# Kernel tuning notes

Measured on AMD Instinct MI355X. Metric: run time of the kernel, lower is better.

Reference implementation:

```python
import jax, jax.numpy as jnp
import numpy as np

B, S, D_IN, D_OUT = 4, 2048, 1024, 1024


def setup_inputs() -> dict:
    key = jax.random.key(0)
    k1, k2, k3, k4 = jax.random.split(key, 4)
    scale = 1.0 / np.sqrt(D_IN)
    return {
        "x": jax.random.normal(k1, (B, S, D_IN), dtype=jnp.float32),
        # torch nn.Linear weights have shape [d_out, d_in]
        "Wq": jax.random.normal(k2, (D_OUT, D_IN), dtype=jnp.float32) * scale,
        "Wk": jax.random.normal(k3, (D_OUT, D_IN), dtype=jnp.float32) * scale,
        "Wv": jax.random.normal(k4, (D_OUT, D_IN), dtype=jnp.float32) * scale,
    }


def reference(x, Wq, Wk, Wv):
    # Linear projections (torch Linear: y = x @ W.T), no bias
    q = jnp.einsum('bsd,od->bso', x, Wq)
    k = jnp.einsum('bsd,od->bso', x, Wk)
    v = jnp.einsum('bsd,od->bso', x, Wv)
    s = q.shape[1]
    scores = jnp.einsum('bqd,bkd->bqk', q, k)  # [B, S, S]
    causal = jnp.tril(jnp.ones((s, s), dtype=bool))  # True = keep
    scores = jnp.where(causal[None], scores, -jnp.inf)
    scale = jnp.asarray(k.shape[-1], scores.dtype) ** 0.5
    weights = jax.nn.softmax(scores / scale, axis=-1)
    return jnp.einsum('bqk,bkd->bqd', weights, v)
```

## Files before the change

kernel.cpp:

```cpp
#include <hip/hip_runtime.h>

#define BATCH 4
#define SEQ   2048
#define DIM   1024
#define MTOT  (BATCH * SEQ)
#define BK    32

typedef __bf16 bf16x8 __attribute__((ext_vector_type(8)));
typedef float  f32x4  __attribute__((ext_vector_type(4)));

__device__ __forceinline__ void gl_lds16(const __bf16* g, __bf16* l) {
    __builtin_amdgcn_global_load_lds(
        (const __attribute__((address_space(1))) void*)g,
        (__attribute__((address_space(3))) void*)l,
        16, 0, 0);
}

__global__ __launch_bounds__(256) void cvt_all_kernel(
    const float* __restrict__ x,  const float* __restrict__ w0,
    const float* __restrict__ w1, const float* __restrict__ w2,
    __bf16* __restrict__ xd, __bf16* __restrict__ d0,
    __bf16* __restrict__ d1, __bf16* __restrict__ d2)
{
    const int bid = blockIdx.x;
    const float* s;
    __bf16* d;
    int base;
    if (bid < 4096)      { s = x;  d = xd; base = bid; }
    else if (bid < 4608) { s = w0; d = d0; base = bid - 4096; }
    else if (bid < 5120) { s = w1; d = d1; base = bid - 4608; }
    else                 { s = w2; d = d2; base = bid - 5120; }
    const int i = (base * 256 + threadIdx.x) * 8;
    const float4 a = *(const float4*)(s + i);
    const float4 b = *(const float4*)(s + i + 4);
    bf16x8 o;
    o[0] = (__bf16)a.x; o[1] = (__bf16)a.y; o[2] = (__bf16)a.z; o[3] = (__bf16)a.w;
    o[4] = (__bf16)b.x; o[5] = (__bf16)b.y; o[6] = (__bf16)b.z; o[7] = (__bf16)b.w;
    *(bf16x8*)(d + i) = o;
}

__device__ __forceinline__ void gemm_core(
    const __bf16* __restrict__ A, size_t lda,
    const __bf16* __restrict__ Bm, size_t ldb,
    int m0, int n0, int kTiles,
    __bf16* lA, __bf16* lB,
    f32x4 (&acc)[4][4])
{
    const int tid  = threadIdx.x;
    const int lane = tid & 63;
    const int wave = tid >> 6;
    const int wm = (wave >> 1) << 6;
    const int wn = (wave & 1) << 6;

#pragma unroll
    for (int i = 0; i < 4; ++i)
#pragma unroll
        for (int j = 0; j < 4; ++j)
            acc[i][j] = (f32x4){0.f, 0.f, 0.f, 0.f};

    for (int kt = 0; kt < kTiles; ++kt) {
        const int k0 = kt << 5;
        __syncthreads();
#pragma unroll
        for (int it = 0; it < 2; ++it) {
            const int f   = tid + (it << 8);
            const int row = f >> 2;
            const int col = (f & 3) << 3;
            gl_lds16(A  + (size_t)(m0 + row) * lda + (size_t)(k0 + col), lA + f * 8);
            gl_lds16(Bm + (size_t)(n0 + row) * ldb + (size_t)(k0 + col), lB + f * 8);
        }
        __syncthreads();

        bf16x8 af[4], bfr[4];
#pragma unroll
        for (int i = 0; i < 4; ++i) {
            af[i]  = *(const bf16x8*)(lA + (size_t)(wm + i * 16 + (lane & 15)) * BK + ((lane >> 4) << 3));
            bfr[i] = *(const bf16x8*)(lB + (size_t)(wn + i * 16 + (lane & 15)) * BK + ((lane >> 4) << 3));
        }
#pragma unroll
        for (int i = 0; i < 4; ++i)
#pragma unroll
            for (int j = 0; j < 4; ++j)
                acc[i][j] = __builtin_amdgcn_mfma_f32_16x16x32_bf16(af[i], bfr[j], acc[i][j], 0, 0, 0);
    }
}

__device__ __forceinline__ void store_tile_bf16(
    f32x4 (&acc)[4][4], __bf16* scratch, bool transpose, float scale,
    __bf16* dst, size_t ldo, size_t r0, size_t c0,
    bool expMask = false, bool diag = false)
{
    const int tid  = threadIdx.x;
    const int lane = tid & 63;
    const int wave = tid >> 6;
    const int wm = (wave >> 1) << 6, wn = (wave & 1) << 6;
    const int quad = lane >> 4;
    const int ln15 = lane & 15;

#pragma unroll
    for (int p = 0; p < 4; ++p) {
        __syncthreads();
        if (!transpose) {
            if (wm == ((p >> 1) << 6)) {
#pragma unroll
                for (int ih = 0; ih < 2; ++ih) {
                    const int i = ((p & 1) << 1) + ih;
                    const int lr = ih * 16 + quad * 4;
#pragma unroll
                    for (int j = 0; j < 4; ++j)
#pragma unroll
                        for (int r = 0; r < 4; ++r) {
                            const int lm = wm + ((p & 1) << 5) + lr + r;
                            const int ln = wn + j * 16 + ln15;
                            float v = acc[i][j][r] * scale;
                            if (expMask) {
                                v = (!diag || ln <= lm) ? __expf(v) : 0.f;
                            }
                            scratch[(lr + r) * 136 + wn + j * 16 + ln15] = (__bf16)v;
                        }
                }
            }
        } else {
            if (wn == ((p >> 1) << 6)) {
#pragma unroll
                for (int jh = 0; jh < 2; ++jh) {
                    const int j = ((p & 1) << 1) + jh;
                    const int lr = jh * 16 + ln15;
#pragma unroll
                    for (int i = 0; i < 4; ++i)
#pragma unroll
                        for (int r = 0; r < 4; ++r)
                            scratch[lr * 136 + wm + i * 16 + quad * 4 + r] =
                                (__bf16)(acc[i][j][r] * scale);
                }
            }
        }
        __syncthreads();
#pragma unroll
        for (int it = 0; it < 2; ++it) {
            const int g   = tid + (it << 8);
            const int row = g >> 4;
            const int col = (g & 15) << 3;
            *(bf16x8*)(dst + (r0 + p * 32 + row) * ldo + c0 + col) =
                *(const bf16x8*)(scratch + row * 136 + col);
        }
    }
}

__global__ __launch_bounds__(256) void qkv_kernel(
    const __bf16* __restrict__ x,
    const __bf16* __restrict__ Wq,
    const __bf16* __restrict__ Wk,
    const __bf16* __restrict__ Wv,
    __bf16* __restrict__ Q, __bf16* __restrict__ Kb, __bf16* __restrict__ Vt)
{
    __shared__ __bf16 smem[8192];
    __bf16* lA = smem;
    __bf16* lB = smem + 128 * BK;
    const int L = blockIdx.x;
    const int c = L & 7;
    const int k = L >> 3;
    const int m0 = ((c << 3) + (k / 24)) << 7;
    const int rr = k % 24;
    const int z  = rr >> 3;
    const int n0 = (rr & 7) << 7;
    const __bf16* W = (z == 0) ? Wq : (z == 1) ? Wk : Wv;

    f32x4 acc[4][4];
    gemm_core(x, DIM, W, DIM, m0, n0, DIM / BK, lA, lB, acc);

    if (z == 0) {
        store_tile_bf16(acc, smem, false, 1.f, Q,  DIM, m0, n0);
    } else if (z == 1) {
        store_tile_bf16(acc, smem, false, 1.f, Kb, DIM, m0, n0);
    } else {
        const size_t b = (size_t)(m0 >> 11), ms0 = (size_t)(m0 & (SEQ - 1));
        store_tile_bf16(acc, smem, true, 1.f, Vt + b * DIM * SEQ, SEQ, n0, ms0);
    }
}

__global__ __launch_bounds__(256) void scores_kernel(
    const __bf16* __restrict__ Q, const __bf16* __restrict__ Kb,
    __bf16* __restrict__ Sc)
{
    const int L = blockIdx.x;
    const int g = (L & 7) * 68 + (L >> 3);
    const int b = g / 136;
    const int t = g - b * 136;
    int i = (int)((sqrtf(8.f * t + 1.f) - 1.f) * 0.5f);
    while ((i + 1) * (i + 2) / 2 <= t) ++i;
    while (i * (i + 1) / 2 > t) --i;
    const int j = t - i * (i + 1) / 2;

    __shared__ __bf16 smem[8192];
    __bf16* lA = smem;
    __bf16* lB = smem + 128 * BK;
    const __bf16* A  = Q  + (size_t)b * SEQ * DIM;
    const __bf16* Bm = Kb + (size_t)b * SEQ * DIM;

    f32x4 acc[4][4];
    gemm_core(A, DIM, Bm, DIM, i << 7, j << 7, DIM / BK, lA, lB, acc);

    store_tile_bf16(acc, smem, false, 0.03125f,
                    Sc + (size_t)b * SEQ * SEQ, SEQ,
                    (size_t)(i << 7), (size_t)(j << 7),
                    true, (i == j));
}

__global__ __launch_bounds__(256) void rowsum_kernel(
    const __bf16* __restrict__ Sc, float* __restrict__ invl)
{
    const int rg = blockIdx.x;
    const int b  = rg >> 11;
    const int r  = rg & (SEQ - 1);
    const __bf16* row = Sc + ((size_t)b * SEQ + r) * SEQ;

    const int tid  = threadIdx.x;
    const int lane = tid & 63;
    const int wv   = tid >> 6;
    const int width = ((r >> 7) + 1) << 7;
    const int c0 = tid << 3;

    float s = 0.f;
    if (c0 < width) {
        const bf16x8 in = *(const bf16x8*)(row + c0);
#pragma unroll
        for (int k = 0; k < 8; ++k) s += (float)in[k];
    }
#pragma unroll
    for (int off = 32; off > 0; off >>= 1)
        s += __shfl_xor(s, off);

    __shared__ float red[4];
    if (lane == 0) red[wv] = s;
    __syncthreads();
    if (tid == 0)
        invl[rg] = 1.f / (red[0] + red[1] + red[2] + red[3]);
}

__global__ __launch_bounds__(256) void pv_kernel(
    const __bf16* __restrict__ P, const __bf16* __restrict__ Vt,
    const float* __restrict__ invl, float* __restrict__ out)
{
    const int L = blockIdx.x;
    const int c = L & 7;
    const int k = L >> 3;
    const int b = c >> 1;
    const int i = 15 - (c & 1) - ((k >> 3) << 1);
    const int x = k & 7;

    __shared__ __bf16 smem[8192];
    __bf16* lA = smem;
    __bf16* lB = smem + 128 * BK;
    const __bf16* A  = P  + (size_t)b * SEQ * SEQ;
    const __bf16* Bm = Vt + (size_t)b * DIM * SEQ;

    f32x4 acc[4][4];
    gemm_core(A, SEQ, Bm, SEQ, i << 7, x << 7, (i + 1) * (128 / BK), lA, lB, acc);

    const int lane = threadIdx.x & 63;
    const int wave = threadIdx.x >> 6;
    const int wm = (wave >> 1) << 6, wn = (wave & 1) << 6;
#pragma unroll
    for (int ii = 0; ii < 4; ++ii)
#pragma unroll
        for (int jj = 0; jj < 4; ++jj)
#pragma unroll
            for (int r = 0; r < 4; ++r) {
                const int m = (i << 7) + wm + ii * 16 + ((lane >> 4) << 2) + r;
                const int n = (x << 7) + wn + jj * 16 + (lane & 15);
                out[((size_t)b * SEQ + m) * DIM + n] =
                    acc[ii][jj][r] * invl[(b << 11) + m];
            }
}

extern "C" void kernel_launch(void* const* d_in, const int* in_sizes, int n_in,
                              void* d_out, int out_size, void* d_ws, size_t ws_size,
                              hipStream_t stream) {
    const float* x  = (const float*)d_in[0];
    const float* Wq = (const float*)d_in[1];
    const float* Wk = (const float*)d_in[2];
    const float* Wv = (const float*)d_in[3];
    float* out = (float*)d_out;

    char* ws = (char*)d_ws;
    __bf16* Q  = (__bf16*)(ws);
    __bf16* Kb = (__bf16*)(ws + (16ull << 20));
    __bf16* Vt = (__bf16*)(ws + (32ull << 20));
    __bf16* Sc = (__bf16*)(ws + (48ull << 20));
    __bf16* Wqb = (__bf16*)(ws + (80ull << 20));
    __bf16* Wkb = (__bf16*)(ws + (82ull << 20));
    __bf16* Wvb = (__bf16*)(ws + (84ull << 20));
    float*  invl = (float*)(ws + (86ull << 20));
    __bf16* xb  = (__bf16*)d_out;

    cvt_all_kernel<<<dim3(5632), 256, 0, stream>>>(x, Wq, Wk, Wv, xb, Wqb, Wkb, Wvb);

    qkv_kernel    <<<dim3(1536), 256, 0, stream>>>(xb, Wqb, Wkb, Wvb, Q, Kb, Vt);
    scores_kernel <<<dim3(544),  256, 0, stream>>>(Q, Kb, Sc);
    rowsum_kernel <<<dim3(MTOT), 256, 0, stream>>>(Sc, invl);
    pv_kernel     <<<dim3(512),  256, 0, stream>>>(Sc, Vt, invl, out);
}
```

Measured before the change: 243.6 us.

## Rewrite QKV projection GEMM with 256x256 tiles, 8 waves, pipelined LDS staging

Replaces the generic 128x128 gemm_core in the QKV projection with a dedicated 256x256-tile kernel using 512 threads and a BK=64 double-buffered LDS pipeline that interleaves global-to-LDS staging of each half-tile with MFMA quarters. It adds an XOR swizzle to reduce LDS bank conflicts, and raises wave priority around the MFMA blocks. Epilogues are rewritten to stage through padded LDS for coalesced bf16x8 stores, including the transposed V layout. Larger tiles cut global/L2 traffic per flop, at the cost of 128KB LDS per block, higher register pressure, and only 384 blocks, which may leave CUs underfilled.

```diff
diff --git a/kernel.cpp b/kernel.cpp
--- a/kernel.cpp
+++ b/kernel.cpp
@@ -7,6 +7,7 @@
 #define BK    32
 
 typedef __bf16 bf16x8 __attribute__((ext_vector_type(8)));
+typedef __bf16 bf16x4 __attribute__((ext_vector_type(4)));
 typedef float  f32x4  __attribute__((ext_vector_type(4)));
 
 __device__ __forceinline__ void gl_lds16(const __bf16* g, __bf16* l) {
@@ -147,35 +148,180 @@
     }
 }
 
-__global__ __launch_bounds__(256) void qkv_kernel(
+__global__ __launch_bounds__(512, 2) void qkv_kernel(
     const __bf16* __restrict__ x,
     const __bf16* __restrict__ Wq,
     const __bf16* __restrict__ Wk,
     const __bf16* __restrict__ Wv,
     __bf16* __restrict__ Q, __bf16* __restrict__ Kb, __bf16* __restrict__ Vt)
 {
-    __shared__ __bf16 smem[8192];
-    __bf16* lA = smem;
-    __bf16* lB = smem + 128 * BK;
-    const int L = blockIdx.x;
-    const int c = L & 7;
-    const int k = L >> 3;
-    const int m0 = ((c << 3) + (k / 24)) << 7;
-    const int rr = k % 24;
-    const int z  = rr >> 3;
-    const int n0 = (rr & 7) << 7;
+    __shared__ __bf16 smem[65536];
+
+    const int L  = blockIdx.x;
+    const int g  = (L & 7) * 48 + (L >> 3);
+    const int z  = g >> 7;
+    const int rm = g & 127;
+    const int m0 = (rm >> 2) << 8;
+    const int n0 = (rm & 3) << 8;
     const __bf16* W = (z == 0) ? Wq : (z == 1) ? Wk : Wv;
 
-    f32x4 acc[4][4];
-    gemm_core(x, DIM, W, DIM, m0, n0, DIM / BK, lA, lB, acc);
-
-    if (z == 0) {
-        store_tile_bf16(acc, smem, false, 1.f, Q,  DIM, m0, n0);
-    } else if (z == 1) {
-        store_tile_bf16(acc, smem, false, 1.f, Kb, DIM, m0, n0);
+    const int tid  = threadIdx.x;
+    const int lane = tid & 63;
+    const int ln15 = lane & 15;
+    const int quad = lane >> 4;
+    const int wave = tid >> 6;
+    const int wm   = wave >> 2;
+    const int wn   = wave & 3;
+
+    const int r0  = tid >> 3;
+    const int cst = ((tid & 7) << 3) ^ ((r0 & 4) ? 16 : 0);
+    const __bf16* Ab = x + (size_t)m0 * DIM;
+    const __bf16* Bb = W + (size_t)n0 * DIM;
+
+    const int qx = (quad << 3) ^ ((ln15 & 4) ? 16 : 0);
+    int aoff[4], boff[2];
+#pragma unroll
+    for (int i = 0; i < 4; ++i) aoff[i] = (wm * 64 + i * 16 + ln15) * 64 + qx;
+#pragma unroll
+    for (int j = 0; j < 2; ++j) boff[j] = (wn * 32 + j * 16 + ln15) * 64 + qx;
+
+    f32x4 acc[8][4];
+#pragma unroll
+    for (int i = 0; i < 8; ++i)
+#pragma unroll
+        for (int j = 0; j < 4; ++j) acc[i][j] = (f32x4){0.f, 0.f, 0.f, 0.f};
+
+#define STAGE_A(h, t) do {                                                    \
+    const __bf16* gs_ = Ab + (size_t)((h) * 128 + r0) * DIM + ((t) << 6) + cst; \
+    __bf16* ls_ = smem + (((t) & 1) * 32768 + (h) * 8192);                    \
+    gl_lds16(gs_, ls_ + tid * 8);                                             \
+    gl_lds16(gs_ + (size_t)64 * DIM, ls_ + tid * 8 + 4096); } while (0)
+#define STAGE_B(h, t) do {                                                    \
+    const __bf16* gs_ = Bb + (size_t)((h) * 128 + r0) * DIM + ((t) << 6) + cst; \
+    __bf16* ls_ = smem + (((t) & 1) * 32768 + 16384 + (h) * 8192);            \
+    gl_lds16(gs_, ls_ + tid * 8);                                             \
+    gl_lds16(gs_ + (size_t)64 * DIM, ls_ + tid * 8 + 4096); } while (0)
+
+    bf16x8 aF[4][2], bF[2][2];
+#define LOAD_A(h) do { const __bf16* p_ = smem + cb_ * 32768 + (h) * 8192;    \
+    _Pragma("unroll") for (int i_ = 0; i_ < 4; ++i_) {                        \
+        aF[i_][0] = *(const bf16x8*)(p_ + aoff[i_]);                          \
+        aF[i_][1] = *(const bf16x8*)(p_ + aoff[i_] + 32); } } while (0)
+#define LOAD_B(h) do { const __bf16* p_ = smem + cb_ * 32768 + 16384 + (h) * 8192; \
+    _Pragma("unroll") for (int j_ = 0; j_ < 2; ++j_) {                        \
+        bF[j_][0] = *(const bf16x8*)(p_ + boff[j_]);                          \
+        bF[j_][1] = *(const bf16x8*)(p_ + boff[j_] + 32); } } while (0)
+#define MFMA_Q(mh, nh) do {                                                   \
+    __builtin_amdgcn_s_setprio(1);                                            \
+    _Pragma("unroll") for (int i_ = 0; i_ < 4; ++i_)                          \
+    _Pragma("unroll") for (int j_ = 0; j_ < 2; ++j_) {                        \
+        acc[(mh)*4+i_][(nh)*2+j_] = __builtin_amdgcn_mfma_f32_16x16x32_bf16(  \
+            aF[i_][0], bF[j_][0], acc[(mh)*4+i_][(nh)*2+j_], 0, 0, 0);        \
+        acc[(mh)*4+i_][(nh)*2+j_] = __builtin_amdgcn_mfma_f32_16x16x32_bf16(  \
+            aF[i_][1], bF[j_][1], acc[(mh)*4+i_][(nh)*2+j_], 0, 0, 0); }      \
+    __builtin_amdgcn_s_setprio(0); } while (0)
+
+    const int nt = DIM / 64;
+
+    STAGE_B(0, 0);
+    STAGE_A(1, 0);
+    STAGE_A(0, 0);
+    STAGE_B(1, 0);
+    STAGE_B(0, 1);
+    STAGE_A(1, 1);
+    asm volatile("s_waitcnt vmcnt(4)" ::: "memory");
+    __builtin_amdgcn_s_barrier();
+
+    for (int T = 0; T < nt; ++T) {
+        const int cb_ = T & 1;
+        LOAD_A(0); LOAD_B(0);
+        if (T + 1 < nt) STAGE_A(0, T + 1);
+        __builtin_amdgcn_s_barrier();
+        MFMA_Q(0, 0);
+        __builtin_amdgcn_s_barrier();
+        LOAD_A(1);
+        if (T + 1 < nt) STAGE_B(1, T + 1);
+        __builtin_amdgcn_s_barrier();
+        MFMA_Q(1, 0);
+        __builtin_amdgcn_s_barrier();
+        LOAD_B(1);
+        if (T + 2 < nt) STAGE_B(0, T + 2);
+        __builtin_amdgcn_s_barrier();
+        MFMA_Q(1, 1);
+        __builtin_amdgcn_s_barrier();
+        LOAD_A(0);
+        if (T + 2 < nt) {
+            STAGE_A(1, T + 2);
+            asm volatile("s_waitcnt vmcnt(4)" ::: "memory");
+        } else if (T + 1 < nt) {
+            asm volatile("s_waitcnt vmcnt(0)" ::: "memory");
+        }
+        __builtin_amdgcn_s_barrier();
+        MFMA_Q(0, 1);
+        __builtin_amdgcn_s_barrier();
+    }
+#undef STAGE_A
+#undef STAGE_B
+#undef LOAD_A
+#undef LOAD_B
+#undef MFMA_Q
+
+    __syncthreads();
+    __bf16* scratch = smem;
+
+    if (z < 2) {
+        __bf16* dst = (z == 0) ? Q : Kb;
+#pragma unroll
+        for (int h = 0; h < 2; ++h) {
+#pragma unroll
+            for (int im = 0; im < 4; ++im) {
+                const int lr = wm * 64 + im * 16 + quad * 4;
+#pragma unroll
+                for (int nf = 0; nf < 4; ++nf) {
+                    const int lc = (nf >> 1) * 128 + wn * 32 + (nf & 1) * 16 + ln15;
+#pragma unroll
+                    for (int r = 0; r < 4; ++r)
+                        scratch[(lr + r) * 264 + lc] = (__bf16)acc[h * 4 + im][nf][r];
+                }
+            }
+            __syncthreads();
+#pragma unroll
+            for (int it = 0; it < 8; ++it) {
+                const int f = tid + (it << 9);
+                const int row = f >> 5, blk = f & 31;
+                *(bf16x8*)(dst + (size_t)(m0 + h * 128 + row) * DIM + n0 + blk * 8) =
+                    *(const bf16x8*)(scratch + row * 264 + blk * 8);
+            }
+            __syncthreads();
+        }
     } else {
-        const size_t b = (size_t)(m0 >> 11), ms0 = (size_t)(m0 & (SEQ - 1));
-        store_tile_bf16(acc, smem, true, 1.f, Vt + b * DIM * SEQ, SEQ, n0, ms0);
+        const size_t b  = (size_t)(m0 >> 11);
+        const int  ms0  = m0 & (SEQ - 1);
+        __bf16* dst = Vt + b * (size_t)DIM * SEQ;
+#pragma unroll
+        for (int h = 0; h < 2; ++h) {
+#pragma unroll
+            for (int jn = 0; jn < 2; ++jn) {
+                const int lrow = wn * 32 + jn * 16 + ln15;
+#pragma unroll
+                for (int mf = 0; mf < 8; ++mf) {
+                    const int lcol = (mf >> 2) * 128 + wm * 64 + (mf & 3) * 16 + quad * 4;
+                    bf16x4 v;
+#pragma unroll
+                    for (int r = 0; r < 4; ++r) v[r] = (__bf16)acc[mf][h * 2 + jn][r];
+                    *(bf16x4*)(scratch + lrow * 264 + lcol) = v;
+                }
+            }
+            __syncthreads();
+#pragma unroll
+            for (int it = 0; it < 8; ++it) {
+                const int f = tid + (it << 9);
+                const int row = f >> 5, blk = f & 31;
+                *(bf16x8*)(dst + (size_t)(n0 + h * 128 + row) * SEQ + ms0 + blk * 8) =
+                    *(const bf16x8*)(scratch + row * 264 + blk * 8);
+            }
+            __syncthreads();
+        }
     }
 }
 
@@ -296,7 +442,7 @@
 
     cvt_all_kernel<<<dim3(5632), 256, 0, stream>>>(x, Wq, Wk, Wv, xb, Wqb, Wkb, Wvb);
 
-    qkv_kernel    <<<dim3(1536), 256, 0, stream>>>(xb, Wqb, Wkb, Wvb, Q, Kb, Vt);
+    qkv_kernel    <<<dim3(384),  512, 0, stream>>>(xb, Wqb, Wkb, Wvb, Q, Kb, Vt);
     scores_kernel <<<dim3(544),  256, 0, stream>>>(Q, Kb, Sc);
     rowsum_kernel <<<dim3(MTOT), 256, 0, stream>>>(Sc, invl);
     pv_kernel     <<<dim3(512),  256, 0, stream>>>(Sc, Vt, invl, out);
```

After: 243.9 us. About the same (+0.1%).

## Double-buffer GEMM core with BK=64 swizzled LDS and fuse rowsum into scores

Applied to the files above, without the earlier changes.

Replaces the single-buffered BK=32 GEMM loop with a double-buffered BK=64 pipeline. It uses XOR-swizzled LDS addressing, explicit vmcnt waits and s_setprio around the MFMA block. The separate rowsum kernel is removed: scores_kernel accumulates the bf16-rounded exp row sums via shuffles and atomics into a buffer that the convert kernel zeroes. The QKV kernel now runs 512 blocks that each compute three 128-wide output tiles, relying on contiguous Wq/Wk/Wv bf16 buffers. This trades more LDS per block and atomic traffic for fewer barriers, better load/compute overlap and one fewer launch.

```diff
diff --git a/kernel.cpp b/kernel.cpp
--- a/kernel.cpp
+++ b/kernel.cpp
@@ -4,10 +4,11 @@
 #define SEQ   2048
 #define DIM   1024
 #define MTOT  (BATCH * SEQ)
-#define BK    32
 
 typedef __bf16 bf16x8 __attribute__((ext_vector_type(8)));
 typedef float  f32x4  __attribute__((ext_vector_type(4)));
+
+#define VMCNT(N) asm volatile("s_waitcnt vmcnt(" #N ")" ::: "memory")
 
 __device__ __forceinline__ void gl_lds16(const __bf16* g, __bf16* l) {
     __builtin_amdgcn_global_load_lds(
@@ -20,9 +21,15 @@
     const float* __restrict__ x,  const float* __restrict__ w0,
     const float* __restrict__ w1, const float* __restrict__ w2,
     __bf16* __restrict__ xd, __bf16* __restrict__ d0,
-    __bf16* __restrict__ d1, __bf16* __restrict__ d2)
+    __bf16* __restrict__ d1, __bf16* __restrict__ d2,
+    float* __restrict__ sums)
 {
     const int bid = blockIdx.x;
+    if (bid >= 5632) {
+        const int i = ((bid - 5632) * 256 + threadIdx.x) * 4;
+        *(float4*)(sums + i) = (float4){0.f, 0.f, 0.f, 0.f};
+        return;
+    }
     const float* s;
     __bf16* d;
     int base;
@@ -39,56 +46,85 @@
     *(bf16x8*)(d + i) = o;
 }
 
-__device__ __forceinline__ void gemm_core(
-    const __bf16* __restrict__ A, size_t lda,
-    const __bf16* __restrict__ Bm, size_t ldb,
-    int m0, int n0, int kTiles,
-    __bf16* lA, __bf16* lB,
-    f32x4 (&acc)[4][4])
+__device__ __forceinline__ void unit128(
+    const __bf16* __restrict__ Ab, size_t lda,
+    const __bf16* __restrict__ Bb, size_t ldb,
+    int nt, __bf16* smem, f32x4 (&acc)[4][4])
 {
     const int tid  = threadIdx.x;
     const int lane = tid & 63;
+    const int ln15 = lane & 15;
+    const int quad = lane >> 4;
     const int wave = tid >> 6;
-    const int wm = (wave >> 1) << 6;
-    const int wn = (wave & 1) << 6;
+    const int wm   = (wave >> 1) << 6;
+    const int wn   = (wave & 1) << 6;
+
+    const int cq = (((quad << 3) + ((ln15 & 7) << 3)) & 63);
+
+    int aoff[4], boff[4];
+#pragma unroll
+    for (int i = 0; i < 4; ++i) aoff[i] = (wm + i * 16 + ln15) * 64 + cq;
+#pragma unroll
+    for (int j = 0; j < 4; ++j) boff[j] = 8192 + (wn + j * 16 + ln15) * 64 + cq;
 
 #pragma unroll
     for (int i = 0; i < 4; ++i)
 #pragma unroll
-        for (int j = 0; j < 4; ++j)
-            acc[i][j] = (f32x4){0.f, 0.f, 0.f, 0.f};
-
-    for (int kt = 0; kt < kTiles; ++kt) {
-        const int k0 = kt << 5;
-        __syncthreads();
-#pragma unroll
-        for (int it = 0; it < 2; ++it) {
-            const int f   = tid + (it << 8);
-            const int row = f >> 2;
-            const int col = (f & 3) << 3;
-            gl_lds16(A  + (size_t)(m0 + row) * lda + (size_t)(k0 + col), lA + f * 8);
-            gl_lds16(Bm + (size_t)(n0 + row) * ldb + (size_t)(k0 + col), lB + f * 8);
-        }
-        __syncthreads();
-
-        bf16x8 af[4], bfr[4];
+        for (int j = 0; j < 4; ++j) acc[i][j] = (f32x4){0.f, 0.f, 0.f, 0.f};
+
+#define STG(t) do {                                                           \
+    const int k0_ = (t) << 6;                                                 \
+    __bf16* lb_ = smem + (((t) & 1) << 14);                                   \
+    _Pragma("unroll") for (int it_ = 0; it_ < 4; ++it_) {                     \
+        const int c_ = tid + (it_ << 8);                                      \
+        const int r_ = c_ >> 3;                                               \
+        const int cc_ = ((((c_ & 7) + 8) - (r_ & 7)) & 7) << 3;               \
+        gl_lds16(Ab + (size_t)r_ * lda + k0_ + cc_, lb_ + c_ * 8);            \
+        gl_lds16(Bb + (size_t)r_ * ldb + k0_ + cc_, lb_ + 8192 + c_ * 8);     \
+    } } while (0)
+
+    bf16x8 aF[4][2], bF[4][2];
+
+    STG(0);
+
+    for (int T = 0; T < nt; ++T) {
+        const __bf16* rb = smem + ((T & 1) << 14);
+        if (T + 1 < nt) {
+            STG(T + 1);
+            VMCNT(8);
+        } else {
+            VMCNT(0);
+        }
+        __builtin_amdgcn_s_barrier();
 #pragma unroll
         for (int i = 0; i < 4; ++i) {
-            af[i]  = *(const bf16x8*)(lA + (size_t)(wm + i * 16 + (lane & 15)) * BK + ((lane >> 4) << 3));
-            bfr[i] = *(const bf16x8*)(lB + (size_t)(wn + i * 16 + (lane & 15)) * BK + ((lane >> 4) << 3));
-        }
-#pragma unroll
-        for (int i = 0; i < 4; ++i)
-#pragma unroll
-            for (int j = 0; j < 4; ++j)
-                acc[i][j] = __builtin_amdgcn_mfma_f32_16x16x32_bf16(af[i], bfr[j], acc[i][j], 0, 0, 0);
+            aF[i][0] = *(const bf16x8*)(rb + aoff[i]);
+            aF[i][1] = *(const bf16x8*)(rb + (aoff[i] ^ 32));
+        }
+#pragma unroll
+        for (int j = 0; j < 4; ++j) {
+            bF[j][0] = *(const bf16x8*)(rb + boff[j]);
+            bF[j][1] = *(const bf16x8*)(rb + (boff[j] ^ 32));
+        }
+        __builtin_amdgcn_s_setprio(1);
+#pragma unroll
+        for (int ks = 0; ks < 2; ++ks)
+#pragma unroll
+            for (int i = 0; i < 4; ++i)
+#pragma unroll
+                for (int j = 0; j < 4; ++j)
+                    acc[i][j] = __builtin_amdgcn_mfma_f32_16x16x32_bf16(
+                        aF[i][ks], bF[j][ks], acc[i][j], 0, 0, 0);
+        __builtin_amdgcn_s_setprio(0);
+        __builtin_amdgcn_s_barrier();
     }
+#undef STG
 }
 
 __device__ __forceinline__ void store_tile_bf16(
     f32x4 (&acc)[4][4], __bf16* scratch, bool transpose, float scale,
     __bf16* dst, size_t ldo, size_t r0, size_t c0,
-    bool expMask = false, bool diag = false)
+    bool expMask = false, bool diag = false, float* sums = nullptr)
 {
     const int tid  = threadIdx.x;
     const int lane = tid & 63;
@@ -107,17 +143,28 @@
                     const int i = ((p & 1) << 1) + ih;
                     const int lr = ih * 16 + quad * 4;
 #pragma unroll
-                    for (int j = 0; j < 4; ++j)
-#pragma unroll
-                        for (int r = 0; r < 4; ++r) {
-                            const int lm = wm + ((p & 1) << 5) + lr + r;
+                    for (int r = 0; r < 4; ++r) {
+                        const int lm = wm + ((p & 1) << 5) + lr + r;
+                        float ps = 0.f;
+#pragma unroll
+                        for (int j = 0; j < 4; ++j) {
                             const int ln = wn + j * 16 + ln15;
                             float v = acc[i][j][r] * scale;
                             if (expMask) {
                                 v = (!diag || ln <= lm) ? __expf(v) : 0.f;
                             }
-                            scratch[(lr + r) * 136 + wn + j * 16 + ln15] = (__bf16)v;
+                            const __bf16 vb = (__bf16)v;
+                            scratch[(lr + r) * 136 + ln] = vb;
+                            ps += (float)vb;
                         }
+                        if (sums) {
+#pragma unroll
+                            for (int off = 1; off < 16; off <<= 1)
+                                ps += __shfl_xor(ps, off);
+                            if (ln15 == 0)
+                                atomicAdd(&sums[r0 + (p << 5) + lr + r], ps);
+                        }
+                    }
                 }
             }
         } else {
@@ -147,42 +194,48 @@
     }
 }
 
-__global__ __launch_bounds__(256) void qkv_kernel(
+__global__ __launch_bounds__(256, 2) void qkv_kernel(
     const __bf16* __restrict__ x,
-    const __bf16* __restrict__ Wq,
-    const __bf16* __restrict__ Wk,
-    const __bf16* __restrict__ Wv,
+    const __bf16* __restrict__ Wall,
     __bf16* __restrict__ Q, __bf16* __restrict__ Kb, __bf16* __restrict__ Vt)
 {
-    __shared__ __bf16 smem[8192];
-    __bf16* lA = smem;
-    __bf16* lB = smem + 128 * BK;
-    const int L = blockIdx.x;
-    const int c = L & 7;
-    const int k = L >> 3;
-    const int m0 = ((c << 3) + (k / 24)) << 7;
-    const int rr = k % 24;
-    const int z  = rr >> 3;
-    const int n0 = (rr & 7) << 7;
-    const __bf16* W = (z == 0) ? Wq : (z == 1) ? Wk : Wv;
-
-    f32x4 acc[4][4];
-    gemm_core(x, DIM, W, DIM, m0, n0, DIM / BK, lA, lB, acc);
-
-    if (z == 0) {
-        store_tile_bf16(acc, smem, false, 1.f, Q,  DIM, m0, n0);
-    } else if (z == 1) {
-        store_tile_bf16(acc, smem, false, 1.f, Kb, DIM, m0, n0);
-    } else {
-        const size_t b = (size_t)(m0 >> 11), ms0 = (size_t)(m0 & (SEQ - 1));
-        store_tile_bf16(acc, smem, true, 1.f, Vt + b * DIM * SEQ, SEQ, n0, ms0);
+    __shared__ __bf16 smem[32768];
+
+    const int L  = blockIdx.x;
+    const int g  = (L & 7) * 64 + (L >> 3);
+    const int m0 = (g >> 3) << 7;
+    const int B3 = g & 7;
+
+    const __bf16* Ab = x + (size_t)m0 * DIM;
+
+    for (int uu = 0; uu < 3; ++uu) {
+        const int u = B3 * 3 + uu;
+        f32x4 acc[4][4];
+        unit128(Ab, DIM, Wall + (size_t)(u << 7) * DIM, DIM, DIM / 64,
+                smem, acc);
+
+        const int z  = u >> 3;
+        const int n0 = (u & 7) << 7;
+        if (z == 0) {
+            store_tile_bf16(acc, smem, false, 1.f, Q,  DIM, m0, n0);
+        } else if (z == 1) {
+            store_tile_bf16(acc, smem, false, 1.f, Kb, DIM, m0, n0);
+        } else {
+            const size_t b  = (size_t)(m0 >> 11);
+            const int  ms0  = m0 & (SEQ - 1);
+            store_tile_bf16(acc, smem, true, 1.f,
+                            Vt + b * (size_t)DIM * SEQ, SEQ, n0, ms0);
+        }
+        __syncthreads();
     }
 }
 
-__global__ __launch_bounds__(256) void scores_kernel(
+__global__ __launch_bounds__(256, 2) void scores_kernel(
     const __bf16* __restrict__ Q, const __bf16* __restrict__ Kb,
-    __bf16* __restrict__ Sc)
-{
+    __bf16* __restrict__ Sc, float* __restrict__ sums)
+{
+    __shared__ __bf16 smem[32768];
+
     const int L = blockIdx.x;
     const int g = (L & 7) * 68 + (L >> 3);
     const int b = g / 136;
@@ -192,86 +245,57 @@
     while (i * (i + 1) / 2 > t) --i;
     const int j = t - i * (i + 1) / 2;
 
-    __shared__ __bf16 smem[8192];
-    __bf16* lA = smem;
-    __bf16* lB = smem + 128 * BK;
-    const __bf16* A  = Q  + (size_t)b * SEQ * DIM;
-    const __bf16* Bm = Kb + (size_t)b * SEQ * DIM;
+    const __bf16* A  = Q  + (size_t)b * SEQ * DIM + (size_t)(i << 7) * DIM;
+    const __bf16* Bm = Kb + (size_t)b * SEQ * DIM + (size_t)(j << 7) * DIM;
 
     f32x4 acc[4][4];
-    gemm_core(A, DIM, Bm, DIM, i << 7, j << 7, DIM / BK, lA, lB, acc);
+    unit128(A, DIM, Bm, DIM, DIM / 64, smem, acc);
 
     store_tile_bf16(acc, smem, false, 0.03125f,
                     Sc + (size_t)b * SEQ * SEQ, SEQ,
                     (size_t)(i << 7), (size_t)(j << 7),
-                    true, (i == j));
-}
-
-__global__ __launch_bounds__(256) void rowsum_kernel(
-    const __bf16* __restrict__ Sc, float* __restrict__ invl)
-{
-    const int rg = blockIdx.x;
-    const int b  = rg >> 11;
-    const int r  = rg & (SEQ - 1);
-    const __bf16* row = Sc + ((size_t)b * SEQ + r) * SEQ;
+                    true, (i == j),
+                    sums + (size_t)b * SEQ);
+}
+
+__global__ __launch_bounds__(256, 2) void pv_kernel(
+    const __bf16* __restrict__ P, const __bf16* __restrict__ Vt,
+    const float* __restrict__ sums, float* __restrict__ out)
+{
+    __shared__ __bf16 smem[32768];
+
+    const int L   = blockIdx.x;
+    const int c   = L & 7;
+    const int idx = L >> 3;
+    const int b   = c >> 1;
+    const int ti  = 15 - (c & 1) - ((idx >> 3) << 1);
+    const int dj  = idx & 7;
+
+    const __bf16* A  = P  + (size_t)b * SEQ * SEQ + (size_t)(ti << 7) * SEQ;
+    const __bf16* Bm = Vt + (size_t)b * DIM * SEQ + (size_t)(dj << 7) * SEQ;
+
+    f32x4 acc[4][4];
+    unit128(A, SEQ, Bm, SEQ, (ti + 1) * 2, smem, acc);
 
     const int tid  = threadIdx.x;
     const int lane = tid & 63;
-    const int wv   = tid >> 6;
-    const int width = ((r >> 7) + 1) << 7;
-    const int c0 = tid << 3;
-
-    float s = 0.f;
-    if (c0 < width) {
-        const bf16x8 in = *(const bf16x8*)(row + c0);
-#pragma unroll
-        for (int k = 0; k < 8; ++k) s += (float)in[k];
-    }
-#pragma unroll
-    for (int off = 32; off > 0; off >>= 1)
-        s += __shfl_xor(s, off);
-
-    __shared__ float red[4];
-    if (lane == 0) red[wv] = s;
-    __syncthreads();
-    if (tid == 0)
-        invl[rg] = 1.f / (red[0] + red[1] + red[2] + red[3]);
-}
-
-__global__ __launch_bounds__(256) void pv_kernel(
-    const __bf16* __restrict__ P, const __bf16* __restrict__ Vt,
-    const float* __restrict__ invl, float* __restrict__ out)
-{
-    const int L = blockIdx.x;
-    const int c = L & 7;
-    const int k = L >> 3;
-    const int b = c >> 1;
-    const int i = 15 - (c & 1) - ((k >> 3) << 1);
-    const int x = k & 7;
-
-    __shared__ __bf16 smem[8192];
-    __bf16* lA = smem;
-    __bf16* lB = smem + 128 * BK;
-    const __bf16* A  = P  + (size_t)b * SEQ * SEQ;
-    const __bf16* Bm = Vt + (size_t)b * DIM * SEQ;
-
-    f32x4 acc[4][4];
-    gemm_core(A, SEQ, Bm, SEQ, i << 7, x << 7, (i + 1) * (128 / BK), lA, lB, acc);
-
-    const int lane = threadIdx.x & 63;
-    const int wave = threadIdx.x >> 6;
-    const int wm = (wave >> 1) << 6, wn = (wave & 1) << 6;
-#pragma unroll
-    for (int ii = 0; ii < 4; ++ii)
-#pragma unroll
-        for (int jj = 0; jj < 4; ++jj)
-#pragma unroll
-            for (int r = 0; r < 4; ++r) {
-                const int m = (i << 7) + wm + ii * 16 + ((lane >> 4) << 2) + r;
-                const int n = (x << 7) + wn + jj * 16 + (lane & 15);
-                out[((size_t)b * SEQ + m) * DIM + n] =
-                    acc[ii][jj][r] * invl[(b << 11) + m];
-            }
+    const int ln15 = lane & 15;
+    const int quad = lane >> 4;
+    const int wave = tid >> 6;
+    const int wm   = (wave >> 1) << 6;
+    const int wn   = (wave & 1) << 6;
+
+#pragma unroll
+    for (int i = 0; i < 4; ++i)
+#pragma unroll
+        for (int r = 0; r < 4; ++r) {
+            const int m = (ti << 7) + wm + i * 16 + quad * 4 + r;
+            const float s = sums[(b << 11) + m];
+            float* orow = out + ((size_t)b * SEQ + m) * DIM + (dj << 7);
+#pragma unroll
+            for (int j = 0; j < 4; ++j)
+                orow[wn + j * 16 + ln15] = acc[i][j][r] / s;
+        }
 }
 
 extern "C" void kernel_launch(void* const* d_in, const int* in_sizes, int n_in,
@@ -291,13 +315,13 @@
     __bf16* Wqb = (__bf16*)(ws + (80ull << 20));
     __bf16* Wkb = (__bf16*)(ws + (82ull << 20));
     __bf16* Wvb = (__bf16*)(ws + (84ull << 20));
-    float*  invl = (float*)(ws + (86ull << 20));
+    float*  sums = (float*)(ws + (86ull << 20));
     __bf16* xb  = (__bf16*)d_out;
 
-    cvt_all_kernel<<<dim3(5632), 256, 0, stream>>>(x, Wq, Wk, Wv, xb, Wqb, Wkb, Wvb);
-
-    qkv_kernel    <<<dim3(1536), 256, 0, stream>>>(xb, Wqb, Wkb, Wvb, Q, Kb, Vt);
-    scores_kernel <<<dim3(544),  256, 0, stream>>>(Q, Kb, Sc);
-    rowsum_kernel <<<dim3(MTOT), 256, 0, stream>>>(Sc, invl);
-    pv_kernel     <<<dim3(512),  256, 0, stream>>>(Sc, Vt, invl, out);
-}
+    cvt_all_kernel<<<dim3(5640), 256, 0, stream>>>(x, Wq, Wk, Wv, xb, Wqb, Wkb, Wvb,
+                                                   sums);
+
+    qkv_kernel    <<<dim3(512),  256, 0, stream>>>(xb, Wqb, Q, Kb, Vt);
+    scores_kernel <<<dim3(544),  256, 0, stream>>>(Q, Kb, Sc, sums);
+    pv_kernel     <<<dim3(512),  256, 0, stream>>>(Sc, Vt, sums, out);
+}
```

Result: faster. 211.0 us (-13.4%).
